# Kernel optimization log

Hardware: AMD Instinct MI355X
Metric: run time of the kernel (lower is better)

## Reference

```python
import jax, jax.numpy as jnp
import numpy as np

B, C, T_TEXT, T_FEAT = 16, 192, 512, 2048
DUR_MAX = 8


def setup_inputs() -> dict:
    key = jax.random.key(0)
    k1, k2 = jax.random.split(key)
    x = jax.random.normal(k1, (B, C, T_TEXT), dtype=jnp.float32)
    w = jax.random.randint(k2, (B, T_TEXT), 0, DUR_MAX, dtype=jnp.int32)
    x_mask = jnp.ones((B, T_TEXT), dtype=jnp.float32)
    y_mask = jnp.ones((B, T_FEAT), dtype=jnp.float32)
    return {"x": x, "w": w, "x_mask": x_mask, "y_mask": y_mask}


def _alignment_path(w, x_mask, t_feat):
    # w: (B, T_text) int durations. Builds one-hot path (B, T_feat, T_text):
    # path[b, j, i] = 1 iff cum_w[i-1] <= j < cum_w[i]
    wm = (w.astype(jnp.float32) * x_mask).astype(jnp.int32)  # mask durations
    cum = jnp.cumsum(wm, axis=-1)                            # (B, T_text)
    frames = jnp.arange(t_feat, dtype=jnp.int32)             # (T_feat,)
    lt = (frames[None, :, None] < cum[:, None, :]).astype(jnp.float32)  # (B, T_feat, T_text)
    # subtract shifted-by-one along text axis -> one-hot per frame
    path = lt - jnp.pad(lt[:, :, :-1], ((0, 0), (0, 0), (1, 0)))
    return path


def reference(x, w, x_mask, y_mask):
    # x: (B, C, T_text) -> (B, C, T_feat)
    t_feat = y_mask.shape[-1]
    path = _alignment_path(w, x_mask, t_feat)                # (B, T_feat, T_text)
    xm = x * x_mask[:, None, :]
    y = jnp.einsum("bci,bji->bcj", xm, path)                 # duplicate by duration
    return y * y_mask[:, None, :]
```

## Files before the change

### kernel.cpp

```cpp
#include <hip/hip_runtime.h>


#define BB 16
#define CC 192
#define T_TEXT 512
#define T_FEAT 2048
#define CH_TILE 3
#define NTILES (CC / CH_TILE)
#define NTHREADS 256

__global__ __launch_bounds__(NTHREADS) void dup_by_dur_fused(
    const float* __restrict__ x, const int* __restrict__ w,
    const float* __restrict__ x_mask, const float* __restrict__ y_mask,
    float* __restrict__ out)
{
    const int t    = threadIdx.x;
    const int b    = blockIdx.x / NTILES;
    const int tile = blockIdx.x % NTILES;

    __shared__ int   swm[T_TEXT];
    __shared__ float sxm[T_TEXT];
    __shared__ int   sp[NTHREADS];
    __shared__ short sidx[T_FEAT];
    __shared__ float sscale[T_FEAT];

    for (int i = t; i < T_TEXT; i += NTHREADS) {
        float wf = (float)w[b * T_TEXT + i];
        float xm = x_mask[b * T_TEXT + i];
        swm[i] = (int)(wf * xm);
        sxm[i] = xm;
    }
    __syncthreads();

    const int wm0 = swm[2 * t];
    const int wm1 = swm[2 * t + 1];
    sp[t] = wm0 + wm1;
    for (int off = 1; off < NTHREADS; off <<= 1) {
        __syncthreads();
        int v = (t >= off) ? sp[t - off] : 0;
        __syncthreads();
        sp[t] += v;
    }
    __syncthreads();
    const int P    = sp[t];
    int end1   = P;
    int end0   = P - wm1;
    int start0 = end0 - wm0;

    for (int j = t; j < T_FEAT; j += NTHREADS) {
        sidx[j] = 0;
        sscale[j] = 0.0f;
    }
    __syncthreads();

    {
        int s0 = min(start0, T_FEAT), e0 = min(end0, T_FEAT);
        float xm0 = sxm[2 * t];
        for (int j = s0; j < e0; ++j) { sidx[j] = (short)(2 * t);     sscale[j] = xm0; }
        int s1 = min(end0, T_FEAT),   e1 = min(end1, T_FEAT);
        float xm1 = sxm[2 * t + 1];
        for (int j = s1; j < e1; ++j) { sidx[j] = (short)(2 * t + 1); sscale[j] = xm1; }
    }
    __syncthreads();

    for (int j4 = t; j4 < T_FEAT / 4; j4 += NTHREADS) {
        int j = j4 * 4;
        float4 ym = *(const float4*)(y_mask + b * T_FEAT + j);
        float4 sc = *(float4*)(sscale + j);
        sc.x *= ym.x; sc.y *= ym.y; sc.z *= ym.z; sc.w *= ym.w;
        *(float4*)(sscale + j) = sc;
    }
    __syncthreads();

    for (int c0 = 0; c0 < CH_TILE; ++c0) {
        const int c = tile * CH_TILE + c0;
        const float* __restrict__ xrow = x + ((size_t)b * CC + c) * T_TEXT;
        float* __restrict__ orow = out + ((size_t)b * CC + c) * T_FEAT;
        for (int j4 = t; j4 < T_FEAT / 4; j4 += NTHREADS) {
            int j = j4 * 4;
            short4 i4 = *(const short4*)(sidx + j);
            float4 s4 = *(const float4*)(sscale + j);
            float4 o;
            o.x = xrow[i4.x] * s4.x;
            o.y = xrow[i4.y] * s4.y;
            o.z = xrow[i4.z] * s4.z;
            o.w = xrow[i4.w] * s4.w;
            *(float4*)(orow + j) = o;
        }
    }
}

extern "C" void kernel_launch(void* const* d_in, const int* in_sizes, int n_in,
                              void* d_out, int out_size, void* d_ws, size_t ws_size,
                              hipStream_t stream) {
    const float* x      = (const float*)d_in[0];
    const int*   w      = (const int*)d_in[1];
    const float* x_mask = (const float*)d_in[2];
    const float* y_mask = (const float*)d_in[3];
    float* out = (float*)d_out;

    dup_by_dur_fused<<<BB * NTILES, NTHREADS, 0, stream>>>(x, w, x_mask, y_mask, out);
}
```

Before: 15.68 us.

## Use wave-shuffle scan and hoist loads to cut block barriers

Replaces the shared-memory Hillis-Steele scan, which needed many barriers, with a wavefront shuffle scan plus a small cross-wave total. All global loads (durations, masks, y_mask) are issued up front with vector loads, and shared zeroing is merged into the same phase. This removes several __syncthreads and extra shared arrays. The output loop is fully unrolled across the three channels so each sidx/sscale read is reused three times. Hardcoded indexing assumes NTHREADS=256 and the fixed sizes.

```diff
diff --git a/kernel.cpp b/kernel.cpp
--- a/kernel.cpp
+++ b/kernel.cpp
@@ -8,6 +8,7 @@
 #define CH_TILE 3
 #define NTILES (CC / CH_TILE)
 #define NTHREADS 256
+#define NWAVES (NTHREADS / 64)
 
 __global__ __launch_bounds__(NTHREADS) void dup_by_dur_fused(
     const float* __restrict__ x, const int* __restrict__ w,
@@ -15,78 +16,84 @@
     float* __restrict__ out)
 {
     const int t    = threadIdx.x;
+    const int lane = t & 63;
+    const int wv   = t >> 6;
     const int b    = blockIdx.x / NTILES;
     const int tile = blockIdx.x % NTILES;
 
-    __shared__ int   swm[T_TEXT];
-    __shared__ float sxm[T_TEXT];
-    __shared__ int   sp[NTHREADS];
+    __shared__ int   wtot[NWAVES];
     __shared__ short sidx[T_FEAT];
     __shared__ float sscale[T_FEAT];
 
-    for (int i = t; i < T_TEXT; i += NTHREADS) {
-        float wf = (float)w[b * T_TEXT + i];
-        float xm = x_mask[b * T_TEXT + i];
-        swm[i] = (int)(wf * xm);
-        sxm[i] = xm;
+    const int2   w2  = *(const int2*)(w + b * T_TEXT + 2 * t);
+    const float2 xm2 = *(const float2*)(x_mask + b * T_TEXT + 2 * t);
+    const float4 ymA = *(const float4*)(y_mask + b * T_FEAT + 4 * t);
+    const float4 ymB = *(const float4*)(y_mask + b * T_FEAT + 1024 + 4 * t);
+
+    const int wm0 = (int)((float)w2.x * xm2.x);
+    const int wm1 = (int)((float)w2.y * xm2.y);
+
+    *(int4*)(sidx + 8 * t) = int4{0, 0, 0, 0};
+    *(float4*)(sscale + 4 * t) = float4{0.f, 0.f, 0.f, 0.f};
+    *(float4*)(sscale + 1024 + 4 * t) = float4{0.f, 0.f, 0.f, 0.f};
+
+    int p = wm0 + wm1;
+    #pragma unroll
+    for (int off = 1; off < 64; off <<= 1) {
+        int v = __shfl_up(p, off);
+        if (lane >= off) p += v;
     }
+    if (lane == 63) wtot[wv] = p;
     __syncthreads();
 
-    const int wm0 = swm[2 * t];
-    const int wm1 = swm[2 * t + 1];
-    sp[t] = wm0 + wm1;
-    for (int off = 1; off < NTHREADS; off <<= 1) {
-        __syncthreads();
-        int v = (t >= off) ? sp[t - off] : 0;
-        __syncthreads();
-        sp[t] += v;
-    }
-    __syncthreads();
-    const int P    = sp[t];
-    int end1   = P;
-    int end0   = P - wm1;
-    int start0 = end0 - wm0;
+    int prefix = 0;
+    #pragma unroll
+    for (int k = 0; k < NWAVES; ++k)
+        if (k < wv) prefix += wtot[k];
+    const int end1   = prefix + p;
+    const int end0   = end1 - wm1;
+    const int start0 = end0 - wm0;
 
-    for (int j = t; j < T_FEAT; j += NTHREADS) {
-        sidx[j] = 0;
-        sscale[j] = 0.0f;
+    {
+        int s0 = min(start0, T_FEAT), e0 = min(end0, T_FEAT);
+        for (int j = s0; j < e0; ++j) { sidx[j] = (short)(2 * t);     sscale[j] = xm2.x; }
+        int s1 = e0,                  e1 = min(end1, T_FEAT);
+        for (int j = s1; j < e1; ++j) { sidx[j] = (short)(2 * t + 1); sscale[j] = xm2.y; }
     }
     __syncthreads();
 
     {
-        int s0 = min(start0, T_FEAT), e0 = min(end0, T_FEAT);
-        float xm0 = sxm[2 * t];
-        for (int j = s0; j < e0; ++j) { sidx[j] = (short)(2 * t);     sscale[j] = xm0; }
-        int s1 = min(end0, T_FEAT),   e1 = min(end1, T_FEAT);
-        float xm1 = sxm[2 * t + 1];
-        for (int j = s1; j < e1; ++j) { sidx[j] = (short)(2 * t + 1); sscale[j] = xm1; }
+        float4 a = *(float4*)(sscale + 4 * t);
+        a.x *= ymA.x; a.y *= ymA.y; a.z *= ymA.z; a.w *= ymA.w;
+        *(float4*)(sscale + 4 * t) = a;
+        float4 c = *(float4*)(sscale + 1024 + 4 * t);
+        c.x *= ymB.x; c.y *= ymB.y; c.z *= ymB.z; c.w *= ymB.w;
+        *(float4*)(sscale + 1024 + 4 * t) = c;
     }
     __syncthreads();
 
-    for (int j4 = t; j4 < T_FEAT / 4; j4 += NTHREADS) {
-        int j = j4 * 4;
-        float4 ym = *(const float4*)(y_mask + b * T_FEAT + j);
-        float4 sc = *(float4*)(sscale + j);
-        sc.x *= ym.x; sc.y *= ym.y; sc.z *= ym.z; sc.w *= ym.w;
-        *(float4*)(sscale + j) = sc;
-    }
-    __syncthreads();
+    const float* __restrict__ xr0 = x + ((size_t)b * CC + tile * CH_TILE + 0) * T_TEXT;
+    const float* __restrict__ xr1 = x + ((size_t)b * CC + tile * CH_TILE + 1) * T_TEXT;
+    const float* __restrict__ xr2 = x + ((size_t)b * CC + tile * CH_TILE + 2) * T_TEXT;
+    float* __restrict__ or0 = out + ((size_t)b * CC + tile * CH_TILE + 0) * T_FEAT;
+    float* __restrict__ or1 = out + ((size_t)b * CC + tile * CH_TILE + 1) * T_FEAT;
+    float* __restrict__ or2 = out + ((size_t)b * CC + tile * CH_TILE + 2) * T_FEAT;
 
-    for (int c0 = 0; c0 < CH_TILE; ++c0) {
-        const int c = tile * CH_TILE + c0;
-        const float* __restrict__ xrow = x + ((size_t)b * CC + c) * T_TEXT;
-        float* __restrict__ orow = out + ((size_t)b * CC + c) * T_FEAT;
-        for (int j4 = t; j4 < T_FEAT / 4; j4 += NTHREADS) {
-            int j = j4 * 4;
-            short4 i4 = *(const short4*)(sidx + j);
-            float4 s4 = *(const float4*)(sscale + j);
-            float4 o;
-            o.x = xrow[i4.x] * s4.x;
-            o.y = xrow[i4.y] * s4.y;
-            o.z = xrow[i4.z] * s4.z;
-            o.w = xrow[i4.w] * s4.w;
-            *(float4*)(orow + j) = o;
-        }
+    #pragma unroll
+    for (int rep = 0; rep < T_FEAT / 4 / NTHREADS; ++rep) {
+        const int j = 4 * (t + rep * NTHREADS);
+        const short4 i4 = *(const short4*)(sidx + j);
+        const float4 s4 = *(const float4*)(sscale + j);
+        float4 o;
+        o.x = xr0[i4.x] * s4.x; o.y = xr0[i4.y] * s4.y;
+        o.z = xr0[i4.z] * s4.z; o.w = xr0[i4.w] * s4.w;
+        *(float4*)(or0 + j) = o;
+        o.x = xr1[i4.x] * s4.x; o.y = xr1[i4.y] * s4.y;
+        o.z = xr1[i4.z] * s4.z; o.w = xr1[i4.w] * s4.w;
+        *(float4*)(or1 + j) = o;
+        o.x = xr2[i4.x] * s4.x; o.y = xr2[i4.y] * s4.y;
+        o.z = xr2[i4.z] * s4.z; o.w = xr2[i4.w] * s4.w;
+        *(float4*)(or2 + j) = o;
     }
 }
 
```

Result: faster. 13.30 us (-15.2%).
